# Performance work log

Hardware: AMD Instinct MI355X
Metric: run time of the kernel (lower is better)

## Reference

```python
import math
import jax, jax.numpy as jnp
import numpy as np

B, N, D = 16, 2048, 256
EPS = 1e-8  # torch cosine_similarity default eps
TAU = 3.0   # gumbel-softmax temperature


def setup_inputs() -> dict:
    key = jax.random.key(0)
    k1, k2 = jax.random.split(key)
    return {
        "LowLevelFeatures": jax.random.normal(k1, (B, 1, N, D), dtype=jnp.float32),
        "HighLevelFeatures": jax.random.normal(k2, (B, 1, N, D), dtype=jnp.float32),
        "batch_size": B,
    }


def _forward(LLF4, HLF4):
    LLF = LLF4[:, 0]  # [B,N,D]
    HLF = HLF4[:, 0]  # [B,N,D]
    b, n, d = LLF.shape
    # pairwise cosine similarity [B,N,N]: matmul + norm-product (same math as
    # torch's broadcast cosine_similarity, without the [B,N,N,D] intermediate)
    dots = jnp.einsum('bnd,bmd->bnm', LLF, HLF)
    nl = jnp.linalg.norm(LLF, axis=-1)  # [B,N]
    nh = jnp.linalg.norm(HLF, axis=-1)  # [B,N]
    sim = dots / jnp.maximum(nl[:, :, None] * nh[:, None, :], EPS)
    sim = sim / math.sqrt(d)
    probs = jax.nn.softmax(sim, axis=1)  # softmax over dim 1 (LLF rows)
    # F.gumbel_softmax(probs, tau=3, hard=True, dim=1): probs act as logits
    u = jax.random.uniform(jax.random.key(42), probs.shape,
                           minval=1e-10, maxval=1.0)
    gumbels = -jnp.log(-jnp.log(u))
    y_soft = jax.nn.softmax((probs + gumbels) / TAU, axis=1)
    idx = jnp.argmax(y_soft, axis=1)  # [B,N]: selected LLF-row n per HLF col m
    # torch.where on the one-hot scans row-major over (b, n, m), so per batch
    # the returned n-indices are the SORTED multiset of selected indices
    sl = jnp.sort(idx, axis=-1)  # [B,N]
    bidx = jnp.arange(b)[:, None]  # [B,1]
    aligned = HLF[bidx, sl]  # gather along dim 1 -> [B,N,D]
    # rowwise cosine similarity between gathered HLF and LLF
    w = jnp.sum(aligned * LLF, axis=-1) / jnp.maximum(
        jnp.linalg.norm(aligned, axis=-1) * nl, EPS)  # [B,N]
    noise = jax.nn.softmax(w / 0.1, axis=1)[:, :, None]  # [B,N,1]
    hlf_new = aligned + LLF * noise
    out = HLF.at[bidx, sl].set(hlf_new)
    return out


def reference(LowLevelFeatures, HighLevelFeatures, batch_size):
    return _forward(LowLevelFeatures, HighLevelFeatures)
```

## Files before the change

kernel.cpp:

```cpp
#include <hip/hip_runtime.h>
#include <math.h>

#define NB 16
#define NN 2048
#define ND 256
#define BNtot (NB*NN)
#define HH 33554432u

#define GF1 768
#define GF2 1280

typedef __attribute__((ext_vector_type(8))) short bf16x8;
typedef __attribute__((ext_vector_type(4))) float f32x4;

__device__ __forceinline__ void gld16(const void* g, void* l){
  __builtin_amdgcn_global_load_lds((const __attribute__((address_space(1))) void*)g,
                                   (__attribute__((address_space(3))) void*)l, 16, 0, 0);
}

__device__ __forceinline__ unsigned rotl(unsigned v, int r){
  return __builtin_amdgcn_alignbit(v, v, 32-r);
}
__device__ __forceinline__ unsigned umaxu(unsigned a, unsigned b){ return a > b ? a : b; }
__device__ __forceinline__ unsigned uminu(unsigned a, unsigned b){ return a < b ? a : b; }

__device__ __forceinline__ float gumbelv(unsigned b, unsigned n, unsigned m){
  unsigned f = (b<<22) | (n<<11) | m;
  unsigned x0 = (b < 8u) ? f : (f - HH);
  unsigned x1 = x0 + HH;
  const unsigned ks0=0u, ks1=42u, ks2=0u^42u^0x1BD11BDAu;
  unsigned v0 = x0 + ks0;
  unsigned v1 = x1 + ks1;
#define TFR(r) { v0 += v1; v1 = rotl(v1,(r)); v1 ^= v0; }
  TFR(13) TFR(15) TFR(26) TFR(6)
  v0 += ks1; v1 += ks2 + 1u;
  TFR(17) TFR(29) TFR(16) TFR(24)
  v0 += ks2; v1 += ks0 + 2u;
  TFR(13) TFR(15) TFR(26) TFR(6)
  v0 += ks0; v1 += ks1 + 3u;
  TFR(17) TFR(29) TFR(16) TFR(24)
  v0 += ks1; v1 += ks2 + 4u;
  TFR(13) TFR(15) TFR(26) TFR(6)
  v0 += ks2; v1 += ks0 + 5u;
#undef TFR
  unsigned bits = (b < 8u) ? v0 : v1;
  float fl = __uint_as_float((bits>>9) | 0x3F800000u) - 1.0f;
  float u = fmaxf(1e-10f, fl + 1e-10f);
  return -logf(-logf(u));
}

__device__ __forceinline__ float gfromkey(unsigned key){
  float fl = __uint_as_float(key | 0x3F800000u) - 1.0f;
  float u = fmaxf(1e-10f, fl + 1e-10f);
  return -logf(-logf(u));
}

__device__ __forceinline__ void gumbel_body(int gb, float* __restrict__ pcv, int* __restrict__ pci){
  int t    = gb*256 + (int)threadIdx.x;
  int half = t & 1;
  int m    = (t >> 1) & 2047;
  int bl   = (t >> 12) & 7;
  int nq   = t >> 15;
  int chunkbase = nq << 7;
  int nstart = chunkbase + (half << 6);
  unsigned x0 = ((unsigned)bl << 22) | ((unsigned)nstart << 11) | (unsigned)m;
  const unsigned KS2 = 42u ^ 0x1BD11BDAu;
  unsigned a1=0, a2=0, c1=0, c2=0;
  unsigned vk = (unsigned)(127 - (half<<6));
#define TFR(r)       { v0 += v1; v1 = rotl(v1,(r)); v1 ^= v0; }
#define TFRI(r, inj) { v0 += v1 + (inj); v1 = rotl(v1,(r)); v1 ^= v0; }
  #pragma unroll 4
  for (int j = 0; j < 64; ++j){
    unsigned v0 = x0;
    unsigned v1 = x0 + (HH + 42u);
    TFR(13) TFR(15) TFR(26) TFR(6)
    v1 += KS2 + 1u;
    TFRI(17, 42u) TFR(29) TFR(16) TFR(24)
    v1 += 2u;
    TFRI(13, KS2) TFR(15) TFR(26) TFR(6)
    v1 += 42u + 3u;
    TFR(17) TFR(29) TFR(16) TFR(24)
    v1 += KS2 + 4u;
    TFRI(13, 42u) TFR(15) TFR(26) TFR(6)
    v0 += KS2; v1 += 5u;
    unsigned pa = (v0 & 0xFFFFFE00u) | vk;
    unsigned pb = (v1 & 0xFFFFFE00u) | vk;
    unsigned ta = uminu(pa, a1);
    a1 = umaxu(pa, a1);
    a2 = umaxu(ta, a2);
    unsigned tc = uminu(pb, c1);
    c1 = umaxu(pb, c1);
    c2 = umaxu(tc, c2);
    x0 += 2048u;
    vk -= 1u;
  }
#undef TFR
#undef TFRI
  unsigned p1 = __shfl_xor((int)a1, 1), p2 = __shfl_xor((int)a2, 1);
  unsigned q1 = __shfl_xor((int)c1, 1), q2 = __shfl_xor((int)c2, 1);
  unsigned A1 = umaxu(a1, p1);
  unsigned A2 = umaxu(uminu(a1, p1), umaxu(a2, p2));
  unsigned C1 = umaxu(c1, q1);
  unsigned C2 = umaxu(uminu(c1, q1), umaxu(c2, q2));
  if (half == 0){
    int baseA = (((nq*NB + bl  )*NN + m) << 1);
    int baseB = (((nq*NB + bl+8)*NN + m) << 1);
    pcv[baseA+0] = gfromkey(A1 >> 9); pci[baseA+0] = chunkbase + 127 - (int)(A1 & 127u);
    pcv[baseA+1] = gfromkey(A2 >> 9); pci[baseA+1] = chunkbase + 127 - (int)(A2 & 127u);
    pcv[baseB+0] = gfromkey(C1 >> 9); pci[baseB+0] = chunkbase + 127 - (int)(C1 & 127u);
    pcv[baseB+1] = gfromkey(C2 >> 9); pci[baseB+1] = chunkbase + 127 - (int)(C2 & 127u);
  }
}

__launch_bounds__(256)
__global__ void kgumbel(float* __restrict__ pcv, int* __restrict__ pci){
  gumbel_body(blockIdx.x, pcv, pci);
}

__global__ void knorms(const float* __restrict__ LLF, const float* __restrict__ HLF,
                       float* __restrict__ nl, float* __restrict__ nh){
  int row = blockIdx.x;
  int wave = threadIdx.x >> 6;
  int lane = threadIdx.x & 63;
  const float* src = wave ? HLF : LLF;
  float4 v = ((const float4*)(src + (size_t)row*ND))[lane];
  float s = v.x*v.x + v.y*v.y + v.z*v.z + v.w*v.w;
  for (int o=32;o;o>>=1) s += __shfl_down(s,o);
  if (lane==0) (wave? nh: nl)[row] = sqrtf(s);
}

__launch_bounds__(256)
__global__ void kfuse1(const float* __restrict__ LLF, const float* __restrict__ HLF,
                       ushort* __restrict__ Abf, ushort* __restrict__ Bbf,
                       float* __restrict__ nl, float* __restrict__ nh,
                       float* __restrict__ pcv, int* __restrict__ pci){
  int bid = blockIdx.x;
  if (bid < GF1){ gumbel_body(GF2 + bid, pcv, pci); return; }
  int pid = bid - GF1;
  int px  = pid & 8191;
  int py  = pid >> 13;
  int w    = threadIdx.x >> 6;
  int lane = threadIdx.x & 63;
  int r = px*4 + w;
  const float* src = py ? HLF : LLF;
  ushort* dst      = py ? Bbf : Abf;
  float4 v = ((const float4*)(src + (size_t)r*ND))[lane];
  float s = v.x*v.x + v.y*v.y + v.z*v.z + v.w*v.w;
  for (int o=32;o;o>>=1) s += __shfl_down(s,o);
  if (lane==0) (py ? nh : nl)[r] = sqrtf(s);
  uint2 u;
  u.x = (__float_as_uint(v.y)&0xFFFF0000u)|(__float_as_uint(v.x)>>16);
  u.y = (__float_as_uint(v.w)&0xFFFF0000u)|(__float_as_uint(v.z)>>16);
  int b = r >> 11, nloc = r & 2047;
  int k = lane << 2;
  int ck = k >> 6;
  int j  = k & 63;
  int qi = j >> 3;
  size_t off = (size_t)b*524288 + (size_t)ck*131072 + (size_t)nloc*64
             + ((qi ^ (nloc & 7)) << 3) + (j & 7);
  *(uint2*)(dst + off) = u;
}

#define K1 0.09016844f
__launch_bounds__(256)
__global__ void kfuse2(const ushort* __restrict__ Abf, const ushort* __restrict__ Bbf,
                       const float* __restrict__ nl, const float* __restrict__ nh,
                       float* __restrict__ partS,
                       float* __restrict__ pcv, int* __restrict__ pci){
  __shared__ ushort As[128*64];
  __shared__ ushort Bs[128*64];
  __shared__ float colsum[128];
  int bid = blockIdx.x;
  int grp = bid / 21, rr = bid % 21;
  if (rr < 5){ gumbel_body(grp*5 + rr, pcv, pci); return; }
  int g  = grp*16 + (rr - 5);
  const int b  = g >> 8;
  const int n0 = ((g >> 4) & 15) << 7;
  const int m0 = (g & 15) << 7;
  const int tid  = threadIdx.x;
  const int lane = tid & 63;
  const int w    = tid >> 6;
  const int wn   = w >> 1, wm = w & 1;
  const int quad = lane >> 4, l15 = lane & 15;
  if (tid < 128) colsum[tid] = 0.0f;

  const ushort* Ab = Abf + (size_t)b*524288;
  const ushort* Bb = Bbf + (size_t)b*524288;

  f32x4 acc[4][4];
  #pragma unroll
  for (int i=0;i<4;i++)
    #pragma unroll
    for (int j=0;j<4;j++) acc[i][j] = (f32x4){0.f,0.f,0.f,0.f};

  for (int ck=0; ck<4; ck++){
    __syncthreads();
    const ushort* ga = Ab + (size_t)ck*131072 + (size_t)n0*64;
    const ushort* gb = Bb + (size_t)ck*131072 + (size_t)m0*64;
    #pragma unroll
    for (int t=0;t<4;t++){
      int seg = (w*4 + t) * 512;
      gld16(ga + seg + lane*8, &As[seg]);
      gld16(gb + seg + lane*8, &Bs[seg]);
    }
    __syncthreads();
    #pragma unroll
    for (int ks=0; ks<64; ks+=32){
      bf16x8 af[4], bf[4];
      #pragma unroll
      for (int t=0;t<4;t++){
        int R = wn*64 + t*16 + l15;
        af[t] = *(const bf16x8*)(&As[R*64 + ((((ks>>3)+quad) ^ (R&7))<<3)]);
      }
      #pragma unroll
      for (int t=0;t<4;t++){
        int R = wm*64 + t*16 + l15;
        bf[t] = *(const bf16x8*)(&Bs[R*64 + ((((ks>>3)+quad) ^ (R&7))<<3)]);
      }
      #pragma unroll
      for (int ti=0;ti<4;ti++)
        #pragma unroll
        for (int tj=0;tj<4;tj++)
          acc[ti][tj] = __builtin_amdgcn_mfma_f32_16x16x32_bf16(af[ti], bf[tj], acc[ti][tj], 0, 0, 0);
    }
  }

  float an[4][4];
  #pragma unroll
  for (int ti=0;ti<4;ti++)
    #pragma unroll
    for (int r=0;r<4;r++)
      an[ti][r] = K1 / nl[b*NN + n0 + wn*64 + ti*16 + quad*4 + r];
  float bm[4];
  #pragma unroll
  for (int tj=0;tj<4;tj++)
    bm[tj] = 1.0f / nh[b*NN + m0 + wm*64 + tj*16 + l15];
  #pragma unroll
  for (int tj=0;tj<4;tj++){
    float s = 0.0f;
    #pragma unroll
    for (int ti=0;ti<4;ti++)
      #pragma unroll
      for (int r=0;r<4;r++)
        s += __builtin_amdgcn_exp2f(acc[ti][tj][r]*an[ti][r]*bm[tj] - K1);
    s += __shfl_down(s, 32);
    s += __shfl_down(s, 16);
    if (lane < 16) atomicAdd(&colsum[wm*64 + tj*16 + l15], s);
  }
  __syncthreads();
  if (tid < 128)
    partS[(size_t)((g >> 4) & 15)*BNtot + b*NN + m0 + tid] = colsum[tid];
}

__launch_bounds__(256)
__global__ void kgemm_mfma(const float* __restrict__ LLF, const float* __restrict__ HLF,
                           const float* __restrict__ nl, const float* __restrict__ nh,
                           float* __restrict__ partS){
  __shared__ ushort As[128][72];
  __shared__ ushort Bs[128][72];
  __shared__ float colsum[128];
  const int b  = blockIdx.z;
  const int n0 = blockIdx.y << 7;
  const int m0 = blockIdx.x << 7;
  const float* Ab = LLF + (size_t)b*NN*ND;
  const float* Bb = HLF + (size_t)b*NN*ND;
  const int tid  = threadIdx.x;
  const int lane = tid & 63;
  const int w    = tid >> 6;
  const int wn   = w >> 1, wm = w & 1;
  const int quad = lane >> 4, l15 = lane & 15;
  if (tid < 128) colsum[tid] = 0.0f;

  f32x4 acc[4][4];
  #pragma unroll
  for (int i=0;i<4;i++)
    #pragma unroll
    for (int j=0;j<4;j++) acc[i][j] = (f32x4){0.f,0.f,0.f,0.f};

  const int rbase = tid >> 3;
  const int kq    = (tid & 7) << 3;

  for (int ck=0; ck<4; ck++){
    const int k0 = ck << 6;
    __syncthreads();
    #pragma unroll
    for (int pi=0; pi<4; pi++){
      int row = rbase + (pi<<5);
      const float* pa = Ab + (size_t)(n0+row)*ND + k0 + kq;
      float4 a0 = *(const float4*)pa;
      float4 a1 = *(const float4*)(pa+4);
      uint4 ua;
      ua.x = (__float_as_uint(a0.y)&0xFFFF0000u)|(__float_as_uint(a0.x)>>16);
      ua.y = (__float_as_uint(a0.w)&0xFFFF0000u)|(__float_as_uint(a0.z)>>16);
      ua.z = (__float_as_uint(a1.y)&0xFFFF0000u)|(__float_as_uint(a1.x)>>16);
      ua.w = (__float_as_uint(a1.w)&0xFFFF0000u)|(__float_as_uint(a1.z)>>16);
      *(uint4*)(&As[row][kq]) = ua;
      const float* pb = Bb + (size_t)(m0+row)*ND + k0 + kq;
      float4 b0 = *(const float4*)pb;
      float4 b1 = *(const float4*)(pb+4);
      uint4 ub;
      ub.x = (__float_as_uint(b0.y)&0xFFFF0000u)|(__float_as_uint(b0.x)>>16);
      ub.y = (__float_as_uint(b0.w)&0xFFFF0000u)|(__float_as_uint(b0.z)>>16);
      ub.z = (__float_as_uint(b1.y)&0xFFFF0000u)|(__float_as_uint(b1.x)>>16);
      ub.w = (__float_as_uint(b1.w)&0xFFFF0000u)|(__float_as_uint(b1.z)>>16);
      *(uint4*)(&Bs[row][kq]) = ub;
    }
    __syncthreads();
    #pragma unroll
    for (int ks=0; ks<64; ks+=32){
      bf16x8 af[4], bf[4];
      #pragma unroll
      for (int t=0;t<4;t++)
        af[t] = *(const bf16x8*)(&As[wn*64 + t*16 + l15][ks + quad*8]);
      #pragma unroll
      for (int t=0;t<4;t++)
        bf[t] = *(const bf16x8*)(&Bs[wm*64 + t*16 + l15][ks + quad*8]);
      #pragma unroll
      for (int ti=0;ti<4;ti++)
        #pragma unroll
        for (int tj=0;tj<4;tj++)
          acc[ti][tj] = __builtin_amdgcn_mfma_f32_16x16x32_bf16(af[ti], bf[tj], acc[ti][tj], 0, 0, 0);
    }
  }

  float an[4][4];
  #pragma unroll
  for (int ti=0;ti<4;ti++)
    #pragma unroll
    for (int r=0;r<4;r++)
      an[ti][r] = K1 / nl[b*NN + n0 + wn*64 + ti*16 + quad*4 + r];
  float bm[4];
  #pragma unroll
  for (int tj=0;tj<4;tj++)
    bm[tj] = 1.0f / nh[b*NN + m0 + wm*64 + tj*16 + l15];
  #pragma unroll
  for (int tj=0;tj<4;tj++){
    float s = 0.0f;
    #pragma unroll
    for (int ti=0;ti<4;ti++)
      #pragma unroll
      for (int r=0;r<4;r++)
        s += __builtin_amdgcn_exp2f(acc[ti][tj][r]*an[ti][r]*bm[tj] - K1);
    s += __shfl_down(s, 32);
    s += __shfl_down(s, 16);
    if (lane < 16) atomicAdd(&colsum[wm*64 + tj*16 + l15], s);
  }
  __syncthreads();
  if (tid < 128)
    partS[(size_t)blockIdx.y*BNtot + b*NN + m0 + tid] = colsum[tid];
}

__launch_bounds__(256)
__global__ void kresolve(const float* __restrict__ LLF, const float* __restrict__ HLF,
                         const float* __restrict__ nl, const float* __restrict__ nh,
                         const float* __restrict__ partS,
                         const float* __restrict__ pcv, const int* __restrict__ pci,
                         int* __restrict__ idx){
  int w    = threadIdx.x >> 6;
  int lane = threadIdx.x & 63;
  int g = blockIdx.x*4 + w;
  int b = g >> 11, m = g & 2047;
  float ps = (lane < 16) ? partS[(size_t)lane*BNtot + g] : 0.0f;
  ps += __shfl_down(ps, 8);
  ps += __shfl_down(ps, 4);
  ps += __shfl_down(ps, 2);
  ps += __shfl_down(ps, 1);
  float invS = 1.0f / __shfl(ps, 0);
  float pv = -INFINITY; int pn = 0;
  if (lane < 32){
    int base = ((((lane>>1)*NB + b)*NN + m) << 1) + (lane & 1);
    pv = pcv[base]; pn = pci[base];
  }
  float gmax = pv;
  for (int o=32;o;o>>=1) gmax = fmaxf(gmax, __shfl_down(gmax,o));
  gmax = __shfl(gmax, 0);
  unsigned long long mask = __ballot(pv >= gmax - 8e-5f);
  mask &= 0xFFFFFFFFull;
  float4 h = ((const float4*)(HLF + (size_t)g*ND))[lane];
  float nhg = nh[g];
  float bestQ = -INFINITY; int bestN = 1<<30;
  while (mask){
    int src = __builtin_ctzll(mask); mask &= mask-1;
    int   n  = __shfl(pn, src);
    float gv = __shfl(pv, src);
    float4 a = ((const float4*)(LLF + ((size_t)b*NN + n)*ND))[lane];
    float d = a.x*h.x + a.y*h.y + a.z*h.z + a.w*h.w;
    for (int o=32;o;o>>=1) d += __shfl_down(d,o);
    d = __shfl(d, 0);
    float sim = (d / fmaxf(nl[b*NN+n]*nhg, 1e-8f)) * 0.0625f;
    float q = expf(sim - 0.0625f)*invS + gv;
    if (q > bestQ || (q == bestQ && n < bestN)){ bestQ = q; bestN = n; }
  }
  if (lane==0) idx[g] = bestN;
}

__launch_bounds__(256)
__global__ void kstats(const float* __restrict__ A, const float* __restrict__ Bm,
                       const float* __restrict__ nl, const float* __restrict__ nh,
                       float* __restrict__ Mout, float* __restrict__ Sinv){
  __shared__ float As[64][33];
  __shared__ float Bs[64][33];
  __shared__ float Cs[64][65];
  const int b  = blockIdx.x >> 5;
  const int m0 = (blockIdx.x & 31) << 6;
  const float* Ab = A  + (size_t)b*NN*ND;
  const float* Bb = Bm + (size_t)b*NN*ND;
  const int tid = threadIdx.x;
  const int tx = tid & 15, ty = tid >> 4;
  float nhv[4];
  #pragma unroll
  for (int j=0;j<4;j++) nhv[j] = nh[b*NN + m0 + tx*4 + j];
  float Mr = -INFINITY, Sr = 0.0f;
  for (int nt=0; nt<NN; nt+=64){
    float acc[4][4] = {{0.f,0.f,0.f,0.f},{0.f,0.f,0.f,0.f},{0.f,0.f,0.f,0.f},{0.f,0.f,0.f,0.f}};
    for (int kc=0; kc<ND; kc+=32){
      __syncthreads();
      #pragma unroll
      for (int s=0;s<2;s++){
        int f = tid + (s<<8);
        int r = f >> 3;
        int c = (f & 7) << 2;
        float4 va = *(const float4*)(Ab + (size_t)(nt+r)*ND + kc + c);
        As[r][c]=va.x; As[r][c+1]=va.y; As[r][c+2]=va.z; As[r][c+3]=va.w;
        float4 vb = *(const float4*)(Bb + (size_t)(m0+r)*ND + kc + c);
        Bs[r][c]=vb.x; Bs[r][c+1]=vb.y; Bs[r][c+2]=vb.z; Bs[r][c+3]=vb.w;
      }
      __syncthreads();
      #pragma unroll 4
      for (int k=0;k<32;k++){
        float a0=As[ty*4+0][k], a1=As[ty*4+1][k], a2=As[ty*4+2][k], a3=As[ty*4+3][k];
        float b0=Bs[tx*4+0][k], b1=Bs[tx*4+1][k], b2=Bs[tx*4+2][k], b3=Bs[tx*4+3][k];
        acc[0][0]+=a0*b0; acc[0][1]+=a0*b1; acc[0][2]+=a0*b2; acc[0][3]+=a0*b3;
        acc[1][0]+=a1*b0; acc[1][1]+=a1*b1; acc[1][2]+=a1*b2; acc[1][3]+=a1*b3;
        acc[2][0]+=a2*b0; acc[2][1]+=a2*b1; acc[2][2]+=a2*b2; acc[2][3]+=a2*b3;
        acc[3][0]+=a3*b0; acc[3][1]+=a3*b1; acc[3][2]+=a3*b2; acc[3][3]+=a3*b3;
      }
    }
    float nlv[4];
    #pragma unroll
    for (int i=0;i<4;i++) nlv[i] = nl[b*NN + nt + ty*4 + i];
    __syncthreads();
    #pragma unroll
    for (int i=0;i<4;i++)
      #pragma unroll
      for (int j=0;j<4;j++){
        float denom = fmaxf(nlv[i]*nhv[j], 1e-8f);
        Cs[ty*4+i][tx*4+j] = (acc[i][j]/denom)*0.0625f;
      }
    __syncthreads();
    if (tid < 64){
      float tmax = -INFINITY;
      #pragma unroll 8
      for (int r=0;r<64;r++) tmax = fmaxf(tmax, Cs[r][tid]);
      float newM = fmaxf(Mr, tmax);
      float s = 0.0f;
      #pragma unroll 4
      for (int r=0;r<64;r++) s += expf(Cs[r][tid]-newM);
      Sr = Sr*expf(Mr-newM) + s;
      Mr = newM;
    }
  }
  if (tid < 64){
    Mout[b*NN+m0+tid] = Mr;
    Sinv[b*NN+m0+tid] = 1.0f/Sr;
  }
}

__launch_bounds__(256)
__global__ void kargmax(const float* __restrict__ A, const float* __restrict__ Bm,
                        const float* __restrict__ nl, const float* __restrict__ nh,
                        const float* __restrict__ Mv, const float* __restrict__ Sv,
                        int* __restrict__ idxout){
  __shared__ float As[64][33];
  __shared__ float Bs[64][33];
  __shared__ float Vs[16][64];
  __shared__ int   Is[16][64];
  const int b  = blockIdx.x >> 5;
  const int m0 = (blockIdx.x & 31) << 6;
  const float* Ab = A  + (size_t)b*NN*ND;
  const float* Bb = Bm + (size_t)b*NN*ND;
  const int tid = threadIdx.x;
  const int tx = tid & 15, ty = tid >> 4;
  float nhv[4], Mj[4], iSj[4];
  #pragma unroll
  for (int j=0;j<4;j++){
    int m = m0 + tx*4 + j;
    nhv[j] = nh[b*NN + m];
    Mj[j]  = Mv[b*NN + m];
    iSj[j] = Sv[b*NN + m];
  }
  float bestV = -INFINITY; int bestN = 0;
  for (int nt=0; nt<NN; nt+=64){
    float acc[4][4] = {{0.f,0.f,0.f,0.f},{0.f,0.f,0.f,0.f},{0.f,0.f,0.f,0.f},{0.f,0.f,0.f,0.f}};
    for (int kc=0; kc<ND; kc+=32){
      __syncthreads();
      #pragma unroll
      for (int s=0;s<2;s++){
        int f = tid + (s<<8);
        int r = f >> 3;
        int c = (f & 7) << 2;
        float4 va = *(const float4*)(Ab + (size_t)(nt+r)*ND + kc + c);
        As[r][c]=va.x; As[r][c+1]=va.y; As[r][c+2]=va.z; As[r][c+3]=va.w;
        float4 vb = *(const float4*)(Bb + (size_t)(m0+r)*ND + kc + c);
        Bs[r][c]=vb.x; Bs[r][c+1]=vb.y; Bs[r][c+2]=vb.z; Bs[r][c+3]=vb.w;
      }
      __syncthreads();
      #pragma unroll 4
      for (int k=0;k<32;k++){
        float a0=As[ty*4+0][k], a1=As[ty*4+1][k], a2=As[ty*4+2][k], a3=As[ty*4+3][k];
        float b0=Bs[tx*4+0][k], b1=Bs[tx*4+1][k], b2=Bs[tx*4+2][k], b3=Bs[tx*4+3][k];
        acc[0][0]+=a0*b0; acc[0][1]+=a0*b1; acc[0][2]+=a0*b2; acc[0][3]+=a0*b3;
        acc[1][0]+=a1*b0; acc[1][1]+=a1*b1; acc[1][2]+=a1*b2; acc[1][3]+=a1*b3;
        acc[2][0]+=a2*b0; acc[2][1]+=a2*b1; acc[2][2]+=a2*b2; acc[2][3]+=a2*b3;
        acc[3][0]+=a3*b0; acc[3][1]+=a3*b1; acc[3][2]+=a3*b2; acc[3][3]+=a3*b3;
      }
    }
    float nlv[4];
    #pragma unroll
    for (int i=0;i<4;i++) nlv[i] = nl[b*NN + nt + ty*4 + i];
    float lv[4]; int li[4];
    #pragma unroll
    for (int j=0;j<4;j++){ lv[j] = -INFINITY; li[j] = 0; }
    #pragma unroll
    for (int i=0;i<4;i++){
      int n = nt + ty*4 + i;
      #pragma unroll
      for (int j=0;j<4;j++){
        float denom = fmaxf(nlv[i]*nhv[j], 1e-8f);
        float sim = (acc[i][j]/denom)*0.0625f;
        float p = expf(sim - Mj[j]) * iSj[j];
        float v = p + gumbelv((unsigned)b, (unsigned)n, (unsigned)(m0 + tx*4 + j));
        if (v > lv[j]) { lv[j] = v; li[j] = n; }
      }
    }
    __syncthreads();
    #pragma unroll
    for (int j=0;j<4;j++){ Vs[ty][tx*4+j]=lv[j]; Is[ty][tx*4+j]=li[j]; }
    __syncthreads();
    if (tid < 64){
      #pragma unroll 4
      for (int t=0;t<16;t++){
        float v = Vs[t][tid];
        if (v > bestV){ bestV = v; bestN = Is[t][tid]; }
      }
    }
  }
  if (tid < 64) idxout[b*NN + m0 + tid] = bestN;
}

__global__ void ksort(const int* __restrict__ idx, int* __restrict__ cntg,
                      int* __restrict__ offg, int* __restrict__ sl){
  __shared__ int c[NN];
  __shared__ int part[256];
  int b = blockIdx.x, tid = threadIdx.x;
  for (int v=tid; v<NN; v+=256) c[v]=0;
  __syncthreads();
  for (int j=tid; j<NN; j+=256) atomicAdd(&c[idx[b*NN+j]], 1);
  __syncthreads();
  int base = tid*8, s=0, lc[8];
  #pragma unroll
  for (int k=0;k<8;k++){ lc[k]=c[base+k]; s+=lc[k]; }
  part[tid]=s; __syncthreads();
  for (int o=1;o<256;o<<=1){
    int v = (tid>=o)? part[tid-o] : 0;
    __syncthreads();
    part[tid]+=v;
    __syncthreads();
  }
  int run = part[tid]-s;
  #pragma unroll
  for (int k=0;k<8;k++){
    int v = base+k;
    cntg[b*NN+v]=lc[k];
    offg[b*NN+v]=run;
    for (int j=0;j<lc[k];j++) sl[b*NN+run+j]=v;
    run += lc[k];
  }
}

__global__ void kw(const float* __restrict__ LLF, const float* __restrict__ HLF,
                   const float* __restrict__ nl, const float* __restrict__ nh,
                   const int* __restrict__ sl, float* __restrict__ w){
  int g = blockIdx.x*4 + (threadIdx.x>>6);
  int lane = threadIdx.x & 63;
  int b = g >> 11;
  int s = sl[g];
  float4 a = ((const float4*)(HLF + ((size_t)b*NN + s)*ND))[lane];
  float4 l = ((const float4*)(LLF + (size_t)g*ND))[lane];
  float d = a.x*l.x + a.y*l.y + a.z*l.z + a.w*l.w;
  for (int o=32;o;o>>=1) d += __shfl_down(d,o);
  if (lane==0){
    float denom = fmaxf(nh[b*NN+s]*nl[g], 1e-8f);
    w[g] = d/denom;
  }
}

__global__ void knoise(const float* __restrict__ w, float* __restrict__ nz){
  int b = blockIdx.x, tid = threadIdx.x;
  __shared__ float sred[4];
  float x[8]; float mx = -INFINITY;
  #pragma unroll
  for (int k=0;k<8;k++){ x[k] = w[b*NN + tid*8 + k] / 0.1f; mx = fmaxf(mx, x[k]); }
  for (int o=32;o;o>>=1) mx = fmaxf(mx, __shfl_down(mx,o));
  mx = __shfl(mx, 0);
  if ((tid&63)==0) sred[tid>>6] = mx;
  __syncthreads();
  mx = fmaxf(fmaxf(sred[0],sred[1]), fmaxf(sred[2],sred[3]));
  __syncthreads();
  float e[8]; float s = 0.f;
  #pragma unroll
  for (int k=0;k<8;k++){ e[k] = expf(x[k]-mx); s += e[k]; }
  for (int o=32;o;o>>=1) s += __shfl_down(s,o);
  s = __shfl(s, 0);
  if ((tid&63)==0) sred[tid>>6] = s;
  __syncthreads();
  s = sred[0]+sred[1]+sred[2]+sred[3];
  #pragma unroll
  for (int k=0;k<8;k++) nz[b*NN + tid*8 + k] = e[k]/s;
}

__global__ void kfinal(const float* __restrict__ LLF, const float* __restrict__ HLF,
                       const int* __restrict__ cnt, const int* __restrict__ off,
                       const float* __restrict__ nz, float* __restrict__ out){
  int row = blockIdx.x;
  int lane = threadIdx.x;
  int b = row >> 11;
  float4 h = ((const float4*)(HLF + (size_t)row*ND))[lane];
  int c = cnt[row];
  if (c > 0){
    int i = off[row] + c - 1;
    float ns = nz[b*NN + i];
    float4 l = ((const float4*)(LLF + ((size_t)(b*NN + i))*ND))[lane];
    h.x += l.x*ns; h.y += l.y*ns; h.z += l.z*ns; h.w += l.w*ns;
  }
  ((float4*)(out + (size_t)row*ND))[lane] = h;
}

extern "C" void kernel_launch(void* const* d_in, const int* in_sizes, int n_in,
                              void* d_out, int out_size, void* d_ws, size_t ws_size,
                              hipStream_t stream){
  const float* LLF = (const float*)d_in[0];
  const float* HLF = (const float*)d_in[1];
  float* out = (float*)d_out;
  float* ws = (float*)d_ws;

  float* nl  = ws;
  float* nh  = ws + 1*(size_t)BNtot;
  float* iS  = ws + 2*(size_t)BNtot;
  int*   idx = (int*)(ws + 3*(size_t)BNtot);
  int*   cnt = (int*)(ws + 4*(size_t)BNtot);
  int*   off = (int*)(ws + 5*(size_t)BNtot);
  int*   sl  = (int*)(ws + 6*(size_t)BNtot);
  float* wv  = ws + 7*(size_t)BNtot;
  float* nz  = ws + 8*(size_t)BNtot;
  float* partS = ws + 9*(size_t)BNtot;
  float* pcv   = partS + 16*(size_t)BNtot;
  int*   pci   = (int*)(pcv + 32*(size_t)BNtot);
  ushort* Abf  = (ushort*)(pci + 32*(size_t)BNtot);
  ushort* Bbf  = Abf + (size_t)BNtot*ND;
  const size_t needBytes1 = (9 + 16 + 32 + 32) * (size_t)BNtot * 4;
  const size_t needBytes2 = needBytes1 + 2 * (size_t)BNtot * ND * 2;

  if (ws_size >= needBytes2){
    hipLaunchKernelGGL(kfuse1,  dim3(GF1 + 16384), dim3(256), 0, stream, LLF, HLF, Abf, Bbf, nl, nh, pcv, pci);
    hipLaunchKernelGGL(kfuse2,  dim3(21*256),      dim3(256), 0, stream, Abf, Bbf, nl, nh, partS, pcv, pci);
    hipLaunchKernelGGL(kresolve,dim3(BNtot/4),     dim3(256), 0, stream, LLF, HLF, nl, nh, partS, pcv, pci, idx);
  } else if (ws_size >= needBytes1){
    hipLaunchKernelGGL(knorms,   dim3(BNtot),      dim3(128), 0, stream, LLF, HLF, nl, nh);
    hipLaunchKernelGGL(kgemm_mfma,dim3(16,16,16),  dim3(256), 0, stream, LLF, HLF, nl, nh, partS);
    hipLaunchKernelGGL(kgumbel,  dim3(2048),       dim3(256), 0, stream, pcv, pci);
    hipLaunchKernelGGL(kresolve, dim3(BNtot/4),    dim3(256), 0, stream, LLF, HLF, nl, nh, partS, pcv, pci, idx);
  } else {
    float* Mv = ws + 9*(size_t)BNtot;
    hipLaunchKernelGGL(knorms,   dim3(BNtot),      dim3(128), 0, stream, LLF, HLF, nl, nh);
    hipLaunchKernelGGL(kstats,   dim3(NB*32),      dim3(256), 0, stream, LLF, HLF, nl, nh, Mv, iS);
    hipLaunchKernelGGL(kargmax,  dim3(NB*32),      dim3(256), 0, stream, LLF, HLF, nl, nh, Mv, iS, idx);
  }

  hipLaunchKernelGGL(ksort,  dim3(NB),      dim3(256), 0, stream, idx, cnt, off, sl);
  hipLaunchKernelGGL(kw,     dim3(BNtot/4), dim3(256), 0, stream, LLF, HLF, nl, nh, sl, wv);
  hipLaunchKernelGGL(knoise, dim3(NB),      dim3(256), 0, stream, wv, nz);
  hipLaunchKernelGGL(kfinal, dim3(BNtot),   dim3(64),  0, stream, LLF, HLF, cnt, off, nz, out);
}
```

Measured before the change: 302.0 us.

## Move all gumbel work into the convert kernel and run a pure GEMM

All gumbel noise blocks now run interleaved inside the bf16 conversion/norm kernel (one gumbel block per eight convert blocks, 2048 total). The GEMM/column-sum kernel becomes a plain 3D-grid kernel with no gumbel work. The intent is to let the memory-bound conversion hide the ALU-heavy gumbel hashing, so the compute-bound MFMA GEMM is not slowed by sharing with it. The risk is a longer first kernel if the gumbel work is not fully hidden. A mask on the packed index bits is also added.

```diff
diff --git a/kernel.cpp b/kernel.cpp
--- a/kernel.cpp
+++ b/kernel.cpp
@@ -6,9 +6,6 @@
 #define ND 256
 #define BNtot (NB*NN)
 #define HH 33554432u
-
-#define GF1 768
-#define GF2 1280
 
 typedef __attribute__((ext_vector_type(8))) short bf16x8;
 typedef __attribute__((ext_vector_type(4))) float f32x4;
@@ -83,8 +80,8 @@
     v1 += KS2 + 4u;
     TFRI(13, 42u) TFR(15) TFR(26) TFR(6)
     v0 += KS2; v1 += 5u;
-    unsigned pa = (v0 & 0xFFFFFE00u) | vk;
-    unsigned pb = (v1 & 0xFFFFFE00u) | vk;
+    unsigned pa = (v0 & 0xFFFFFE00u) | (vk & 0x1FFu);
+    unsigned pb = (v1 & 0xFFFFFE00u) | (vk & 0x1FFu);
     unsigned ta = uminu(pa, a1);
     a1 = umaxu(pa, a1);
     a2 = umaxu(ta, a2);
@@ -135,23 +132,24 @@
                        float* __restrict__ nl, float* __restrict__ nh,
                        float* __restrict__ pcv, int* __restrict__ pci){
   int bid = blockIdx.x;
-  if (bid < GF1){ gumbel_body(GF2 + bid, pcv, pci); return; }
-  int pid = bid - GF1;
+  int g = bid / 9, r = bid - g*9;
+  if (r == 0){ gumbel_body(g, pcv, pci); return; }
+  int pid = g*8 + (r-1);
   int px  = pid & 8191;
   int py  = pid >> 13;
   int w    = threadIdx.x >> 6;
   int lane = threadIdx.x & 63;
-  int r = px*4 + w;
+  int row = px*4 + w;
   const float* src = py ? HLF : LLF;
   ushort* dst      = py ? Bbf : Abf;
-  float4 v = ((const float4*)(src + (size_t)r*ND))[lane];
+  float4 v = ((const float4*)(src + (size_t)row*ND))[lane];
   float s = v.x*v.x + v.y*v.y + v.z*v.z + v.w*v.w;
   for (int o=32;o;o>>=1) s += __shfl_down(s,o);
-  if (lane==0) (py ? nh : nl)[r] = sqrtf(s);
+  if (lane==0) (py ? nh : nl)[row] = sqrtf(s);
   uint2 u;
   u.x = (__float_as_uint(v.y)&0xFFFF0000u)|(__float_as_uint(v.x)>>16);
   u.y = (__float_as_uint(v.w)&0xFFFF0000u)|(__float_as_uint(v.z)>>16);
-  int b = r >> 11, nloc = r & 2047;
+  int b = row >> 11, nloc = row & 2047;
   int k = lane << 2;
   int ck = k >> 6;
   int j  = k & 63;
@@ -163,20 +161,15 @@
 
 #define K1 0.09016844f
 __launch_bounds__(256)
-__global__ void kfuse2(const ushort* __restrict__ Abf, const ushort* __restrict__ Bbf,
-                       const float* __restrict__ nl, const float* __restrict__ nh,
-                       float* __restrict__ partS,
-                       float* __restrict__ pcv, int* __restrict__ pci){
+__global__ void kgemm_dma(const ushort* __restrict__ Abf, const ushort* __restrict__ Bbf,
+                          const float* __restrict__ nl, const float* __restrict__ nh,
+                          float* __restrict__ partS){
   __shared__ ushort As[128*64];
   __shared__ ushort Bs[128*64];
   __shared__ float colsum[128];
-  int bid = blockIdx.x;
-  int grp = bid / 21, rr = bid % 21;
-  if (rr < 5){ gumbel_body(grp*5 + rr, pcv, pci); return; }
-  int g  = grp*16 + (rr - 5);
-  const int b  = g >> 8;
-  const int n0 = ((g >> 4) & 15) << 7;
-  const int m0 = (g & 15) << 7;
+  const int b  = blockIdx.z;
+  const int n0 = blockIdx.y << 7;
+  const int m0 = blockIdx.x << 7;
   const int tid  = threadIdx.x;
   const int lane = tid & 63;
   const int w    = tid >> 6;
@@ -249,7 +242,7 @@
   }
   __syncthreads();
   if (tid < 128)
-    partS[(size_t)((g >> 4) & 15)*BNtot + b*NN + m0 + tid] = colsum[tid];
+    partS[(size_t)blockIdx.y*BNtot + b*NN + m0 + tid] = colsum[tid];
 }
 
 __launch_bounds__(256)
@@ -662,9 +655,9 @@
   const size_t needBytes2 = needBytes1 + 2 * (size_t)BNtot * ND * 2;
 
   if (ws_size >= needBytes2){
-    hipLaunchKernelGGL(kfuse1,  dim3(GF1 + 16384), dim3(256), 0, stream, LLF, HLF, Abf, Bbf, nl, nh, pcv, pci);
-    hipLaunchKernelGGL(kfuse2,  dim3(21*256),      dim3(256), 0, stream, Abf, Bbf, nl, nh, partS, pcv, pci);
-    hipLaunchKernelGGL(kresolve,dim3(BNtot/4),     dim3(256), 0, stream, LLF, HLF, nl, nh, partS, pcv, pci, idx);
+    hipLaunchKernelGGL(kfuse1,  dim3(18432),     dim3(256), 0, stream, LLF, HLF, Abf, Bbf, nl, nh, pcv, pci);
+    hipLaunchKernelGGL(kgemm_dma,dim3(16,16,16), dim3(256), 0, stream, Abf, Bbf, nl, nh, partS);
+    hipLaunchKernelGGL(kresolve,dim3(BNtot/4),   dim3(256), 0, stream, LLF, HLF, nl, nh, partS, pcv, pci, idx);
   } else if (ws_size >= needBytes1){
     hipLaunchKernelGGL(knorms,   dim3(BNtot),      dim3(128), 0, stream, LLF, HLF, nl, nh);
     hipLaunchKernelGGL(kgemm_mfma,dim3(16,16,16),  dim3(256), 0, stream, LLF, HLF, nl, nh, partS);
```

Result: slower. 312.9 us (+3.6%).
